# Performance work log

Hardware: AMD Instinct MI355X
Metric: run time of the kernel (lower is better)

## Reference

```python
import jax, jax.numpy as jnp
import numpy as np

EPS = 1e-6

def l2norm(x):
    return x / jnp.maximum(jnp.linalg.norm(x, axis=-1, keepdims=True), 1e-12)

def setup_inputs() -> dict:
    key = jax.random.key(0)
    ks = jax.random.split(key, 16)
    B, V, L = 64, 197, 64
    Dv, Dt, E = 768, 768, 256
    s = (2.0 / E) ** 0.5  # kaiming fan_out scale
    inp = {
        'visual_cls': jax.random.normal(ks[0], (B, Dv), jnp.float32),
        'textual_cls': jax.random.normal(ks[1], (B, Dt), jnp.float32),
        'visual_tokens': jax.random.normal(ks[2], (B, V, Dv), jnp.float32),
        'textual_tokens': jax.random.normal(ks[3], (B, L, Dt), jnp.float32),
        'text_length': jnp.maximum(jax.random.randint(ks[4], (B,), 0, L, jnp.int32), 1),
        'Wv': jax.random.normal(ks[5], (Dv, E), jnp.float32) * s,
        'bv': jnp.zeros((E,), jnp.float32),
        'Wt': jax.random.normal(ks[6], (Dt, E), jnp.float32) * s,
        'bt': jnp.zeros((E,), jnp.float32),
        'Wvt': jax.random.normal(ks[7], (Dv, E), jnp.float32) * s,
        'bvt': jnp.zeros((E,), jnp.float32),
        'Wtt': jax.random.normal(ks[8], (Dt, E), jnp.float32) * s,
        'btt': jnp.zeros((E,), jnp.float32),
    }
    return inp

def reference(visual_cls, textual_cls, visual_tokens, textual_tokens, text_length,
              Wv, bv, Wt, bt, Wvt, bvt, Wtt, btt):
    # cls projections
    v_cls = visual_cls @ Wv + bv            # [B, E]
    t_cls = textual_cls @ Wt + bt           # [B, E]
    # token projections + l2 normalize
    v_tok = l2norm(visual_tokens @ Wvt + bvt)   # [B, V, E]
    t_tok = l2norm(textual_tokens @ Wtt + btt)  # [B, L, E]
    B, V, E = v_tok.shape
    L = t_tok.shape[1]
    # full cross-modal token similarity (this is the kernel target)
    sim = jnp.einsum('bvd,qtd->bqvt', v_tok, t_tok)  # [B, Q, V, T]
    # image->text: max over text tokens, plain mean over visual tokens
    image_to_text = jnp.max(sim, axis=-1)            # [B, Q, V]
    image_to_text_sim = jnp.sum(image_to_text, axis=-1) / V  # [B, Q]
    # text->image: max over visual tokens, masked mean over text tokens
    text_to_image = jnp.max(sim, axis=-2)            # [B, Q, T]
    # faithful to original: mask indexed by FIRST batch axis b
    mask = jnp.arange(L)[None, :] >= text_length[:, None]   # [B, T]
    mask3 = mask[:, None, :]                                 # [B, 1, T]
    numer = jnp.sum(jnp.where(mask3, 0.0, text_to_image), axis=-1)
    denom = jnp.maximum(jnp.sum(~mask3, axis=-1).astype(text_to_image.dtype), EPS)
    text_to_image_sim = numer / denom                # [B, Q]
    return (v_cls, t_cls, image_to_text_sim, text_to_image_sim)
```

## Files before the change

kernel.cpp:

```cpp
#include <hip/hip_runtime.h>
#include <hip/hip_bf16.h>

#define NB 64
#define NV 197
#define NL 64
#define ND 768
#define NE 256

typedef __attribute__((ext_vector_type(8))) short bh8;
typedef __attribute__((ext_vector_type(16))) float f32x16;

__device__ inline ushort f2bf(float x) {
  __hip_bfloat16 h = __float2bfloat16(x);
  return *reinterpret_cast<ushort*>(&h);
}

__device__ inline bh8 cvt8(float4 a, float4 b) {
  union { bh8 v; ushort u[8]; } r;
  r.u[0] = f2bf(a.x); r.u[1] = f2bf(a.y); r.u[2] = f2bf(a.z); r.u[3] = f2bf(a.w);
  r.u[4] = f2bf(b.x); r.u[5] = f2bf(b.y); r.u[6] = f2bf(b.z); r.u[7] = f2bf(b.w);
  return r.v;
}

__global__ __launch_bounds__(256) void wcvt_kernel(
    const float* __restrict__ W0, const float* __restrict__ W1,
    const float* __restrict__ W2, const float* __restrict__ W3,
    ushort* __restrict__ O0, ushort* __restrict__ O1,
    ushort* __restrict__ O2, ushort* __restrict__ O3) {
  const float* Win; ushort* Wout;
  switch (blockIdx.y) {
    case 0: Win = W0; Wout = O0; break;
    case 1: Win = W1; Wout = O1; break;
    case 2: Win = W2; Wout = O2; break;
    default: Win = W3; Wout = O3; break;
  }
  const int tk = blockIdx.x % 12, tn = blockIdx.x / 12;
  const int k0 = tk * 64, n0 = tn * 64;
  __shared__ ushort ts[64][72];
  const int tid = threadIdx.x;
#pragma unroll
  for (int i = 0; i < 4; ++i) {
    const int kl = (tid >> 4) + i * 16;
    const int nl = (tid & 15) * 4;
    float4 v = *(const float4*)&Win[(size_t)(k0 + kl) * NE + n0 + nl];
    ts[nl + 0][kl] = f2bf(v.x);
    ts[nl + 1][kl] = f2bf(v.y);
    ts[nl + 2][kl] = f2bf(v.z);
    ts[nl + 3][kl] = f2bf(v.w);
  }
  __syncthreads();
  const int r = tid >> 2, c0 = (tid & 3) * 16;
  bh8 v0 = *(const bh8*)&ts[r][c0];
  bh8 v1 = *(const bh8*)&ts[r][c0 + 8];
  *(bh8*)&Wout[(size_t)(n0 + r) * ND + k0 + c0] = v0;
  *(bh8*)&Wout[(size_t)(n0 + r) * ND + k0 + c0 + 8] = v1;
}

__global__ __launch_bounds__(128, 2) void proj_kernel(
    const float* __restrict__ Xv, const float* __restrict__ Xt,
    const float* __restrict__ Xcv, const float* __restrict__ Xct,
    const ushort* __restrict__ Wvt_t, const ushort* __restrict__ Wtt_t,
    const ushort* __restrict__ Wv_t, const ushort* __restrict__ Wt_t,
    const float* __restrict__ bvt, const float* __restrict__ btt,
    const float* __restrict__ bv, const float* __restrict__ bt,
    ushort* __restrict__ v_tok, ushort* __restrict__ t_tok,
    float* __restrict__ v_cls, float* __restrict__ t_cls) {
  __shared__ float ssq_lds[2][32];

  const int blk = blockIdx.x;
  const float* X; const ushort* W; const float* bias;
  ushort* outb = nullptr; float* outf = nullptr;
  int row0; bool norm;
  if (blk < 394)      { X = Xv;  W = Wvt_t; bias = bvt; outb = v_tok; row0 = blk * 32;         norm = true; }
  else if (blk < 522) { X = Xt;  W = Wtt_t; bias = btt; outb = t_tok; row0 = (blk - 394) * 32; norm = true; }
  else if (blk < 524) { X = Xcv; W = Wv_t;  bias = bv;  outf = v_cls; row0 = (blk - 522) * 32; norm = false; }
  else                { X = Xct; W = Wt_t;  bias = bt;  outf = t_cls; row0 = (blk - 524) * 32; norm = false; }

  const int tid = threadIdx.x;
  const int l = tid & 63, w = tid >> 6;
  const int lr = l & 31, hi = l >> 5;

  const float*  Arow = X + (size_t)(row0 + lr) * ND + hi * 8;
  const ushort* B0 = W + (size_t)(w * 128 + lr) * ND + hi * 8;
  const ushort* B1 = B0 + 32 * ND;
  const ushort* B2 = B0 + 64 * ND;
  const ushort* B3 = B0 + 96 * ND;

  f32x16 acc0 = {0}, acc1 = {0}, acc2 = {0}, acc3 = {0};

#pragma unroll 4
  for (int ks = 0; ks < 48; ++ks) {
    float4 a0 = *(const float4*)(Arow + ks * 16);
    float4 a1 = *(const float4*)(Arow + ks * 16 + 4);
    bh8 b0 = *(const bh8*)(B0 + ks * 16);
    bh8 b1 = *(const bh8*)(B1 + ks * 16);
    bh8 b2 = *(const bh8*)(B2 + ks * 16);
    bh8 b3 = *(const bh8*)(B3 + ks * 16);
    bh8 af = cvt8(a0, a1);
    acc0 = __builtin_amdgcn_mfma_f32_32x32x16_bf16(af, b0, acc0, 0, 0, 0);
    acc1 = __builtin_amdgcn_mfma_f32_32x32x16_bf16(af, b1, acc1, 0, 0, 0);
    acc2 = __builtin_amdgcn_mfma_f32_32x32x16_bf16(af, b2, acc2, 0, 0, 0);
    acc3 = __builtin_amdgcn_mfma_f32_32x32x16_bf16(af, b3, acc3, 0, 0, 0);
  }

  const float bn0 = bias[w * 128 + lr];
  const float bn1 = bias[w * 128 + 32 + lr];
  const float bn2 = bias[w * 128 + 64 + lr];
  const float bn3 = bias[w * 128 + 96 + lr];
#pragma unroll
  for (int r = 0; r < 16; ++r) {
    acc0[r] += bn0; acc1[r] += bn1; acc2[r] += bn2; acc3[r] += bn3;
  }

  if (norm) {
    float p[16];
#pragma unroll
    for (int r = 0; r < 16; ++r)
      p[r] = acc0[r] * acc0[r] + acc1[r] * acc1[r] +
             acc2[r] * acc2[r] + acc3[r] * acc3[r];
#pragma unroll
    for (int off = 1; off < 32; off <<= 1) {
#pragma unroll
      for (int r = 0; r < 16; ++r) p[r] += __shfl_xor(p[r], off);
    }
    if (lr == 0) {
#pragma unroll
      for (int r = 0; r < 16; ++r)
        ssq_lds[w][(r & 3) + 8 * (r >> 2) + 4 * hi] = p[r];
    }
    __syncthreads();
#pragma unroll
    for (int r = 0; r < 16; ++r) {
      const int R = (r & 3) + 8 * (r >> 2) + 4 * hi;
      const float s = ssq_lds[0][R] + ssq_lds[1][R];
      const float scale = 1.0f / fmaxf(sqrtf(s), 1e-12f);
      ushort* orow = outb + (size_t)(row0 + R) * NE + w * 128 + lr;
      orow[0]  = f2bf(acc0[r] * scale);
      orow[32] = f2bf(acc1[r] * scale);
      orow[64] = f2bf(acc2[r] * scale);
      orow[96] = f2bf(acc3[r] * scale);
    }
  } else {
#pragma unroll
    for (int r = 0; r < 16; ++r) {
      const int R = (r & 3) + 8 * (r >> 2) + 4 * hi;
      float* orow = outf + (size_t)(row0 + R) * NE + w * 128 + lr;
      orow[0]  = acc0[r];
      orow[32] = acc1[r];
      orow[64] = acc2[r];
      orow[96] = acc3[r];
    }
  }
}

__global__ __launch_bounds__(256, 2) void sim_kernel(
    const __hip_bfloat16* __restrict__ vt,
    const __hip_bfloat16* __restrict__ tt,
    const int* __restrict__ tlen,
    float* __restrict__ out_i2t,
    float* __restrict__ out_t2i) {
  __shared__ float red[8][4][64];
  __shared__ float wsum[8][4];

  const int blk = blockIdx.x;
  const int q = blk & 63;
  const int bc = blk >> 6;
  const int tid = threadIdx.x;
  const int l = tid & 63;
  const int w = tid >> 6;
  const int lr = l & 31;
  const int hi = l >> 5;
  const size_t bstride = (size_t)NV * NE;

  bh8 breg0[16], breg1[16];
  {
    const __hip_bfloat16* T0 = tt + ((size_t)(q * NL) + lr) * NE + hi * 8;
    const __hip_bfloat16* T1 = T0 + 32 * NE;
#pragma unroll
    for (int s = 0; s < 16; ++s) {
      breg0[s] = *(const bh8*)(T0 + s * 16);
      breg1[s] = *(const bh8*)(T1 + s * 16);
    }
  }

  const int r0 = 32 * w + lr;
  const int r1 = min(128 + 32 * w + lr, NV - 1);

  const __hip_bfloat16* A0 = vt + (size_t)(bc * 8) * bstride + (size_t)r0 * NE + hi * 8;
  const __hip_bfloat16* A1 = vt + (size_t)(bc * 8) * bstride + (size_t)r1 * NE + hi * 8;

  bh8 a0[4], a1[4];
#pragma unroll
  for (int s = 0; s < 4; ++s) {
    a0[s] = *(const bh8*)(A0 + s * 16);
    a1[s] = *(const bh8*)(A1 + s * 16);
  }

  for (int ib = 0; ib < 8; ++ib) {
    f32x16 acc00 = {0}, acc01 = {0}, acc10 = {0}, acc11 = {0};

    __builtin_amdgcn_s_setprio(1);
#pragma unroll
    for (int s = 0; s < 16; ++s) {
      bh8 va0 = a0[s & 3], va1 = a1[s & 3];
      const int sn = s + 4;
      const size_t off = (size_t)(sn & 15) * 16 + (size_t)(sn >> 4) * bstride;
      a0[s & 3] = *(const bh8*)(A0 + off);
      a1[s & 3] = *(const bh8*)(A1 + off);
      acc00 = __builtin_amdgcn_mfma_f32_32x32x16_bf16(va0, breg0[s], acc00, 0, 0, 0);
      acc01 = __builtin_amdgcn_mfma_f32_32x32x16_bf16(va0, breg1[s], acc01, 0, 0, 0);
      acc10 = __builtin_amdgcn_mfma_f32_32x32x16_bf16(va1, breg0[s], acc10, 0, 0, 0);
      acc11 = __builtin_amdgcn_mfma_f32_32x32x16_bf16(va1, breg1[s], acc11, 0, 0, 0);
    }
    __builtin_amdgcn_s_setprio(0);
    A0 += bstride;
    A1 += bstride;

    float i2t_sum = 0.0f;
#pragma unroll
    for (int r = 0; r < 16; ++r) {
      {
        float m = fmaxf(acc00[r], acc01[r]);
        m = fmaxf(m, __shfl_xor(m, 1));
        m = fmaxf(m, __shfl_xor(m, 2));
        m = fmaxf(m, __shfl_xor(m, 4));
        m = fmaxf(m, __shfl_xor(m, 8));
        m = fmaxf(m, __shfl_xor(m, 16));
        i2t_sum += m;
      }
      {
        float m = fmaxf(acc10[r], acc11[r]);
        m = fmaxf(m, __shfl_xor(m, 1));
        m = fmaxf(m, __shfl_xor(m, 2));
        m = fmaxf(m, __shfl_xor(m, 4));
        m = fmaxf(m, __shfl_xor(m, 8));
        m = fmaxf(m, __shfl_xor(m, 16));
        const int row = 128 + 32 * w + (r & 3) + 8 * (r >> 2) + 4 * hi;
        if (row < NV) i2t_sum += m;
      }
    }
    i2t_sum += __shfl_xor(i2t_sum, 32);
    if (l == 0) wsum[ib][w] = i2t_sum;

    float vm0 = -1e30f, vm1 = -1e30f;
#pragma unroll
    for (int r = 0; r < 16; ++r) {
      vm0 = fmaxf(vm0, fmaxf(acc00[r], acc10[r]));
      vm1 = fmaxf(vm1, fmaxf(acc01[r], acc11[r]));
    }
    vm0 = fmaxf(vm0, __shfl_xor(vm0, 32));
    vm1 = fmaxf(vm1, __shfl_xor(vm1, 32));
    if (hi == 0) red[ib][w][lr] = vm0;
    else         red[ib][w][32 + lr] = vm1;
  }

  __syncthreads();

#pragma unroll
  for (int j = 0; j < 2; ++j) {
    const int ib = w * 2 + j;
    const int b = bc * 8 + ib;
    const int len = tlen[b];
    float m = fmaxf(fmaxf(red[ib][0][l], red[ib][1][l]),
                    fmaxf(red[ib][2][l], red[ib][3][l]));
    float v = (l < len) ? m : 0.0f;
#pragma unroll
    for (int off = 1; off < 64; off <<= 1) v += __shfl_xor(v, off);
    if (l == 0) {
      out_t2i[b * NB + q] = v / fmaxf((float)len, 1e-6f);
      out_i2t[b * NB + q] = (wsum[ib][0] + wsum[ib][1] +
                             wsum[ib][2] + wsum[ib][3]) / (float)NV;
    }
  }
}

extern "C" void kernel_launch(void* const* d_in, const int* in_sizes, int n_in,
                              void* d_out, int out_size, void* d_ws, size_t ws_size,
                              hipStream_t stream) {
  (void)in_sizes; (void)n_in; (void)out_size; (void)ws_size;
  const float* visual_cls    = (const float*)d_in[0];
  const float* textual_cls   = (const float*)d_in[1];
  const float* visual_tokens = (const float*)d_in[2];
  const float* textual_tokens= (const float*)d_in[3];
  const int*   text_length   = (const int*)d_in[4];
  const float* Wv  = (const float*)d_in[5];
  const float* bv  = (const float*)d_in[6];
  const float* Wt  = (const float*)d_in[7];
  const float* bt  = (const float*)d_in[8];
  const float* Wvt = (const float*)d_in[9];
  const float* bvt = (const float*)d_in[10];
  const float* Wtt = (const float*)d_in[11];
  const float* btt = (const float*)d_in[12];

  float* out   = (float*)d_out;
  float* v_cls = out;
  float* t_cls = out + NB * NE;
  float* i2t   = out + 2 * NB * NE;
  float* t2i   = i2t + NB * NB;

  ushort* wsb   = (ushort*)d_ws;
  ushort* v_tok = wsb;
  ushort* t_tok = v_tok + (size_t)NB * NV * NE;
  ushort* Wvt_t = t_tok + (size_t)NB * NL * NE;
  ushort* Wtt_t = Wvt_t + (size_t)NE * ND;
  ushort* Wv_t  = Wtt_t + (size_t)NE * ND;
  ushort* Wt_t  = Wv_t  + (size_t)NE * ND;

  wcvt_kernel<<<dim3(48, 4), 256, 0, stream>>>(Wvt, Wtt, Wv, Wt,
                                               Wvt_t, Wtt_t, Wv_t, Wt_t);
  proj_kernel<<<526, 128, 0, stream>>>(visual_tokens, textual_tokens,
                                       visual_cls, textual_cls,
                                       Wvt_t, Wtt_t, Wv_t, Wt_t,
                                       bvt, btt, bv, bt,
                                       v_tok, t_tok, v_cls, t_cls);
  sim_kernel<<<NB * NB / 8, 256, 0, stream>>>((const __hip_bfloat16*)v_tok,
                                              (const __hip_bfloat16*)t_tok,
                                              text_length, i2t, t2i);
}
```

Baseline: 237.7 us.

## Prepack weights in MFMA fragment order, stage activations in LDS, halve sim batch

The weight conversion kernel now writes bf16 weights pre-swizzled into MFMA B-fragment order, so projection lanes load contiguous 16-byte fragments. The projection kernel moves to 64-row tiles with 4 waves, stages fp32 activations through a swizzled LDS buffer with register prefetch of the next chunk, and reuses each weight fragment across two row groups. The similarity kernel handles 4 batches per block instead of 8, doubling grid size for better occupancy at the cost of reloading the text fragments more often.

```diff
diff --git a/kernel.cpp b/kernel.cpp
--- a/kernel.cpp
+++ b/kernel.cpp
@@ -34,79 +34,102 @@
     case 2: Win = W2; Wout = O2; break;
     default: Win = W3; Wout = O3; break;
   }
-  const int tk = blockIdx.x % 12, tn = blockIdx.x / 12;
-  const int k0 = tk * 64, n0 = tn * 64;
-  __shared__ ushort ts[64][72];
-  const int tid = threadIdx.x;
-#pragma unroll
-  for (int i = 0; i < 4; ++i) {
-    const int kl = (tid >> 4) + i * 16;
-    const int nl = (tid & 15) * 4;
-    float4 v = *(const float4*)&Win[(size_t)(k0 + kl) * NE + n0 + nl];
-    ts[nl + 0][kl] = f2bf(v.x);
-    ts[nl + 1][kl] = f2bf(v.y);
-    ts[nl + 2][kl] = f2bf(v.z);
-    ts[nl + 3][kl] = f2bf(v.w);
-  }
-  __syncthreads();
-  const int r = tid >> 2, c0 = (tid & 3) * 16;
-  bh8 v0 = *(const bh8*)&ts[r][c0];
-  bh8 v1 = *(const bh8*)&ts[r][c0 + 8];
-  *(bh8*)&Wout[(size_t)(n0 + r) * ND + k0 + c0] = v0;
-  *(bh8*)&Wout[(size_t)(n0 + r) * ND + k0 + c0 + 8] = v1;
-}
-
-__global__ __launch_bounds__(128, 2) void proj_kernel(
+  const int ks = blockIdx.x;
+  const int t = threadIdx.x;
+  const int l = t & 63;
+  const int lr = l & 31, hi = l >> 5;
+  const int kbase = ks * 16 + hi * 8;
+#pragma unroll
+  for (int i = 0; i < 2; ++i) {
+    const int nt = (t >> 6) + i * 4;
+    const int n = nt * 32 + lr;
+    union { bh8 v; ushort u[8]; } f;
+#pragma unroll
+    for (int e = 0; e < 8; ++e)
+      f.u[e] = f2bf(Win[(size_t)(kbase + e) * NE + n]);
+    *(bh8*)&Wout[(size_t)((nt * 48 + ks) * 64 + l) * 8] = f.v;
+  }
+}
+
+__device__ inline int aswz(int row, int cbyte) {
+  return ((row * 256 + cbyte) ^ ((row & 15) << 4)) >> 2;
+}
+
+__global__ __launch_bounds__(256, 2) void proj_kernel(
     const float* __restrict__ Xv, const float* __restrict__ Xt,
     const float* __restrict__ Xcv, const float* __restrict__ Xct,
-    const ushort* __restrict__ Wvt_t, const ushort* __restrict__ Wtt_t,
-    const ushort* __restrict__ Wv_t, const ushort* __restrict__ Wt_t,
+    const ushort* __restrict__ Fv, const ushort* __restrict__ Ft,
+    const ushort* __restrict__ Fcv, const ushort* __restrict__ Fct,
     const float* __restrict__ bvt, const float* __restrict__ btt,
     const float* __restrict__ bv, const float* __restrict__ bt,
     ushort* __restrict__ v_tok, ushort* __restrict__ t_tok,
     float* __restrict__ v_cls, float* __restrict__ t_cls) {
-  __shared__ float ssq_lds[2][32];
+  __shared__ float a_lds[64 * 64];
+  __shared__ float ssq_lds[2][2][32];
 
   const int blk = blockIdx.x;
-  const float* X; const ushort* W; const float* bias;
+  const float* X; const ushort* F; const float* bias;
   ushort* outb = nullptr; float* outf = nullptr;
   int row0; bool norm;
-  if (blk < 394)      { X = Xv;  W = Wvt_t; bias = bvt; outb = v_tok; row0 = blk * 32;         norm = true; }
-  else if (blk < 522) { X = Xt;  W = Wtt_t; bias = btt; outb = t_tok; row0 = (blk - 394) * 32; norm = true; }
-  else if (blk < 524) { X = Xcv; W = Wv_t;  bias = bv;  outf = v_cls; row0 = (blk - 522) * 32; norm = false; }
-  else                { X = Xct; W = Wt_t;  bias = bt;  outf = t_cls; row0 = (blk - 524) * 32; norm = false; }
-
-  const int tid = threadIdx.x;
-  const int l = tid & 63, w = tid >> 6;
+  if (blk < 197)       { X = Xv;  F = Fv;  bias = bvt; outb = v_tok; row0 = blk * 64;         norm = true; }
+  else if (blk < 261)  { X = Xt;  F = Ft;  bias = btt; outb = t_tok; row0 = (blk - 197) * 64; norm = true; }
+  else if (blk == 261) { X = Xcv; F = Fcv; bias = bv;  outf = v_cls; row0 = 0;                norm = false; }
+  else                 { X = Xct; F = Fct; bias = bt;  outf = t_cls; row0 = 0;                norm = false; }
+
+  const int t = threadIdx.x;
+  const int l = t & 63, w = t >> 6;
   const int lr = l & 31, hi = l >> 5;
-
-  const float*  Arow = X + (size_t)(row0 + lr) * ND + hi * 8;
-  const ushort* B0 = W + (size_t)(w * 128 + lr) * ND + hi * 8;
-  const ushort* B1 = B0 + 32 * ND;
-  const ushort* B2 = B0 + 64 * ND;
-  const ushort* B3 = B0 + 96 * ND;
+  const int wr = w & 1, wc = w >> 1;
+
+  const int srow = t >> 2;
+  const int scq = t & 3;
+  const float* Xrow = X + (size_t)(row0 + srow) * ND;
+
+  const int arow = wr * 32 + lr;
+  const ushort* Fw = F + ((size_t)(wc * 4 * 48) * 64 + l) * 8;
 
   f32x16 acc0 = {0}, acc1 = {0}, acc2 = {0}, acc3 = {0};
 
-#pragma unroll 4
-  for (int ks = 0; ks < 48; ++ks) {
-    float4 a0 = *(const float4*)(Arow + ks * 16);
-    float4 a1 = *(const float4*)(Arow + ks * 16 + 4);
-    bh8 b0 = *(const bh8*)(B0 + ks * 16);
-    bh8 b1 = *(const bh8*)(B1 + ks * 16);
-    bh8 b2 = *(const bh8*)(B2 + ks * 16);
-    bh8 b3 = *(const bh8*)(B3 + ks * 16);
-    bh8 af = cvt8(a0, a1);
-    acc0 = __builtin_amdgcn_mfma_f32_32x32x16_bf16(af, b0, acc0, 0, 0, 0);
-    acc1 = __builtin_amdgcn_mfma_f32_32x32x16_bf16(af, b1, acc1, 0, 0, 0);
-    acc2 = __builtin_amdgcn_mfma_f32_32x32x16_bf16(af, b2, acc2, 0, 0, 0);
-    acc3 = __builtin_amdgcn_mfma_f32_32x32x16_bf16(af, b3, acc3, 0, 0, 0);
-  }
-
-  const float bn0 = bias[w * 128 + lr];
-  const float bn1 = bias[w * 128 + 32 + lr];
-  const float bn2 = bias[w * 128 + 64 + lr];
-  const float bn3 = bias[w * 128 + 96 + lr];
+  float4 g0, g1, g2, g3, n0, n1, n2, n3;
+#define GLOAD(d0, d1, d2, d3, kc) \
+  d0 = *(const float4*)(Xrow + (kc) + scq * 4); \
+  d1 = *(const float4*)(Xrow + (kc) + 16 + scq * 4); \
+  d2 = *(const float4*)(Xrow + (kc) + 32 + scq * 4); \
+  d3 = *(const float4*)(Xrow + (kc) + 48 + scq * 4);
+
+  GLOAD(g0, g1, g2, g3, 0)
+  for (int c = 0; c < 12; ++c) {
+    if (c) __syncthreads();
+    *(float4*)&a_lds[aswz(srow, scq * 16)]       = g0;
+    *(float4*)&a_lds[aswz(srow, 64 + scq * 16)]  = g1;
+    *(float4*)&a_lds[aswz(srow, 128 + scq * 16)] = g2;
+    *(float4*)&a_lds[aswz(srow, 192 + scq * 16)] = g3;
+    if (c < 11) { GLOAD(n0, n1, n2, n3, (c + 1) * 64) }
+    __syncthreads();
+
+#pragma unroll
+    for (int ksl = 0; ksl < 4; ++ksl) {
+      const int ks = c * 4 + ksl;
+      float4 af0 = *(const float4*)&a_lds[aswz(arow, ksl * 64 + hi * 32)];
+      float4 af1 = *(const float4*)&a_lds[aswz(arow, ksl * 64 + hi * 32 + 16)];
+      bh8 b0 = *(const bh8*)(Fw + (size_t)(0 * 48 + ks) * 64 * 8);
+      bh8 b1 = *(const bh8*)(Fw + (size_t)(1 * 48 + ks) * 64 * 8);
+      bh8 b2 = *(const bh8*)(Fw + (size_t)(2 * 48 + ks) * 64 * 8);
+      bh8 b3 = *(const bh8*)(Fw + (size_t)(3 * 48 + ks) * 64 * 8);
+      bh8 af = cvt8(af0, af1);
+      acc0 = __builtin_amdgcn_mfma_f32_32x32x16_bf16(af, b0, acc0, 0, 0, 0);
+      acc1 = __builtin_amdgcn_mfma_f32_32x32x16_bf16(af, b1, acc1, 0, 0, 0);
+      acc2 = __builtin_amdgcn_mfma_f32_32x32x16_bf16(af, b2, acc2, 0, 0, 0);
+      acc3 = __builtin_amdgcn_mfma_f32_32x32x16_bf16(af, b3, acc3, 0, 0, 0);
+    }
+    g0 = n0; g1 = n1; g2 = n2; g3 = n3;
+  }
+#undef GLOAD
+
+  const float bn0 = bias[wc * 128 + lr];
+  const float bn1 = bias[wc * 128 + 32 + lr];
+  const float bn2 = bias[wc * 128 + 64 + lr];
+  const float bn3 = bias[wc * 128 + 96 + lr];
 #pragma unroll
   for (int r = 0; r < 16; ++r) {
     acc0[r] += bn0; acc1[r] += bn1; acc2[r] += bn2; acc3[r] += bn3;
@@ -126,15 +149,15 @@
     if (lr == 0) {
 #pragma unroll
       for (int r = 0; r < 16; ++r)
-        ssq_lds[w][(r & 3) + 8 * (r >> 2) + 4 * hi] = p[r];
+        ssq_lds[wc][wr][(r & 3) + 8 * (r >> 2) + 4 * hi] = p[r];
     }
     __syncthreads();
 #pragma unroll
     for (int r = 0; r < 16; ++r) {
       const int R = (r & 3) + 8 * (r >> 2) + 4 * hi;
-      const float s = ssq_lds[0][R] + ssq_lds[1][R];
+      const float s = ssq_lds[0][wr][R] + ssq_lds[1][wr][R];
       const float scale = 1.0f / fmaxf(sqrtf(s), 1e-12f);
-      ushort* orow = outb + (size_t)(row0 + R) * NE + w * 128 + lr;
+      ushort* orow = outb + (size_t)(row0 + wr * 32 + R) * NE + wc * 128 + lr;
       orow[0]  = f2bf(acc0[r] * scale);
       orow[32] = f2bf(acc1[r] * scale);
       orow[64] = f2bf(acc2[r] * scale);
@@ -144,7 +167,7 @@
 #pragma unroll
     for (int r = 0; r < 16; ++r) {
       const int R = (r & 3) + 8 * (r >> 2) + 4 * hi;
-      float* orow = outf + (size_t)(row0 + R) * NE + w * 128 + lr;
+      float* orow = outf + (size_t)(row0 + wr * 32 + R) * NE + wc * 128 + lr;
       orow[0]  = acc0[r];
       orow[32] = acc1[r];
       orow[64] = acc2[r];
@@ -159,8 +182,8 @@
     const int* __restrict__ tlen,
     float* __restrict__ out_i2t,
     float* __restrict__ out_t2i) {
-  __shared__ float red[8][4][64];
-  __shared__ float wsum[8][4];
+  __shared__ float red[4][4][64];
+  __shared__ float wsum[4][4];
 
   const int blk = blockIdx.x;
   const int q = blk & 63;
@@ -186,8 +209,8 @@
   const int r0 = 32 * w + lr;
   const int r1 = min(128 + 32 * w + lr, NV - 1);
 
-  const __hip_bfloat16* A0 = vt + (size_t)(bc * 8) * bstride + (size_t)r0 * NE + hi * 8;
-  const __hip_bfloat16* A1 = vt + (size_t)(bc * 8) * bstride + (size_t)r1 * NE + hi * 8;
+  const __hip_bfloat16* A0 = vt + (size_t)(bc * 4) * bstride + (size_t)r0 * NE + hi * 8;
+  const __hip_bfloat16* A1 = vt + (size_t)(bc * 4) * bstride + (size_t)r1 * NE + hi * 8;
 
   bh8 a0[4], a1[4];
 #pragma unroll
@@ -196,7 +219,7 @@
     a1[s] = *(const bh8*)(A1 + s * 16);
   }
 
-  for (int ib = 0; ib < 8; ++ib) {
+  for (int ib = 0; ib < 4; ++ib) {
     f32x16 acc00 = {0}, acc01 = {0}, acc10 = {0}, acc11 = {0};
 
     __builtin_amdgcn_s_setprio(1);
@@ -256,10 +279,9 @@
 
   __syncthreads();
 
-#pragma unroll
-  for (int j = 0; j < 2; ++j) {
-    const int ib = w * 2 + j;
-    const int b = bc * 8 + ib;
+  {
+    const int ib = w;
+    const int b = bc * 4 + ib;
     const int len = tlen[b];
     float m = fmaxf(fmaxf(red[ib][0][l], red[ib][1][l]),
                     fmaxf(red[ib][2][l], red[ib][3][l]));
@@ -301,19 +323,19 @@
   ushort* wsb   = (ushort*)d_ws;
   ushort* v_tok = wsb;
   ushort* t_tok = v_tok + (size_t)NB * NV * NE;
-  ushort* Wvt_t = t_tok + (size_t)NB * NL * NE;
-  ushort* Wtt_t = Wvt_t + (size_t)NE * ND;
-  ushort* Wv_t  = Wtt_t + (size_t)NE * ND;
-  ushort* Wt_t  = Wv_t  + (size_t)NE * ND;
+  ushort* Fv    = t_tok + (size_t)NB * NL * NE;
+  ushort* Ft    = Fv + (size_t)8 * 48 * 64 * 8;
+  ushort* Fcv   = Ft + (size_t)8 * 48 * 64 * 8;
+  ushort* Fct   = Fcv + (size_t)8 * 48 * 64 * 8;
 
   wcvt_kernel<<<dim3(48, 4), 256, 0, stream>>>(Wvt, Wtt, Wv, Wt,
-                                               Wvt_t, Wtt_t, Wv_t, Wt_t);
-  proj_kernel<<<526, 128, 0, stream>>>(visual_tokens, textual_tokens,
+                                               Fv, Ft, Fcv, Fct);
+  proj_kernel<<<263, 256, 0, stream>>>(visual_tokens, textual_tokens,
                                        visual_cls, textual_cls,
-                                       Wvt_t, Wtt_t, Wv_t, Wt_t,
+                                       Fv, Ft, Fcv, Fct,
                                        bvt, btt, bv, bt,
                                        v_tok, t_tok, v_cls, t_cls);
-  sim_kernel<<<NB * NB / 8, 256, 0, stream>>>((const __hip_bfloat16*)v_tok,
+  sim_kernel<<<NB * NB / 4, 256, 0, stream>>>((const __hip_bfloat16*)v_tok,
                                               (const __hip_bfloat16*)t_tok,
                                               text_length, i2t, t2i);
 }
```

After: 234.2 us. About the same (-1.4%).
